# Performance work log

Hardware: AMD Instinct MI355X
Metric: run time of the kernel (lower is better)

## Reference

```python
import jax, jax.numpy as jnp
import numpy as np

N_NODES = 100000
N_EDGES = 1600000
D_IN = 128
D_HID = 128
D_OUT = 64
N_LAYERS = 3
BN_EPS = 1e-5


def _mlp_block(h, W1, b1, g, be, W2, b2):
    # PyG MLP([c_in, h, h]): Linear -> BatchNorm -> ReLU -> Linear (plain last)
    h = h @ W1 + b1                      # [N, h]
    mu = jnp.mean(h, axis=0)
    var = jnp.var(h, axis=0)             # biased var, BN training-mode stats
    h = (h - mu) * jax.lax.rsqrt(var + BN_EPS) * g + be
    h = jax.nn.relu(h)
    return h @ W2 + b2


def setup_inputs() -> dict:
    key = jax.random.key(0)
    ks = jax.random.split(key, 16)
    s_in = 1.0 / np.sqrt(D_IN)
    s_h = 1.0 / np.sqrt(D_HID)
    x = jax.random.normal(ks[0], (N_NODES, D_IN), dtype=jnp.float32)
    edge_index = jax.random.randint(ks[1], (2, N_EDGES), 0, N_NODES, dtype=jnp.int64)
    return {
        "x": x,
        "edge_index": edge_index,
        # stacked per-conv MLP params (all layers are 128->128->128)
        "W1": jax.random.normal(ks[2], (N_LAYERS, D_IN, D_HID), jnp.float32) * s_in,
        "b1": jnp.zeros((N_LAYERS, D_HID), jnp.float32),
        "g1": jnp.ones((N_LAYERS, D_HID), jnp.float32),
        "be1": jnp.zeros((N_LAYERS, D_HID), jnp.float32),
        "W2": jax.random.normal(ks[3], (N_LAYERS, D_HID, D_HID), jnp.float32) * s_h,
        "b2": jnp.zeros((N_LAYERS, D_HID), jnp.float32),
        # final MLP([h, h, out])
        "fW1": jax.random.normal(ks[4], (D_HID, D_HID), jnp.float32) * s_h,
        "fb1": jnp.zeros((D_HID,), jnp.float32),
        "fg1": jnp.ones((D_HID,), jnp.float32),
        "fbe1": jnp.zeros((D_HID,), jnp.float32),
        "fW2": jax.random.normal(ks[5], (D_HID, D_OUT), jnp.float32) * s_h,
        "fb2": jnp.zeros((D_OUT,), jnp.float32),
    }


def reference(x, edge_index, W1, b1, g1, be1, W2, b2, fW1, fb1, fg1, fbe1, fW2, fb2):
    src, dst = edge_index[0], edge_index[1]
    for l in range(N_LAYERS):
        # GINConv, eps=0: nn((1+eps)*x + sum_{j->i} x_j)
        aggr = jax.ops.segment_sum(x[src], dst, num_segments=N_NODES)  # [N, d]
        h = x + aggr
        x = jax.nn.relu(_mlp_block(h, W1[l], b1[l], g1[l], be1[l], W2[l], b2[l]))
    # final MLP (dropout=0.5 is identity in eval mode)
    return _mlp_block(x, fW1, fb1, fg1, fbe1, fW2, fb2)
```

## Files before the change

kernel.cpp:

```cpp
#include <hip/hip_runtime.h>
#include <hip/hip_cooperative_groups.h>

namespace cg = cooperative_groups;

#define NN 100000
#define NE 1600000
#define DD 128
#define CAP 56
#define NGROUP 256

static __device__ __forceinline__ unsigned short f2b(float f) {
  unsigned int x = __float_as_uint(f);
  unsigned int r = x + 0x7fffu + ((x >> 16) & 1u);
  return (unsigned short)(r >> 16);
}
static __device__ __forceinline__ float b2f(unsigned short u) {
  return __uint_as_float(((unsigned int)u) << 16);
}

typedef __attribute__((ext_vector_type(8))) short short8;
typedef __attribute__((ext_vector_type(4))) float f32x4;

union V8 {
  uint4 u4;
  short8 s8;
  unsigned short us[8];
};

__global__ void detect_k(const int* __restrict__ ei, int* __restrict__ flag) {
  int v = ei[2 * threadIdx.x + 1];
  unsigned long long b = __ballot(v != 0);
  if (threadIdx.x == 0) *flag = (b == 0ull) ? 1 : 0;
}

__global__ __launch_bounds__(256) void castpack_k(const float* __restrict__ x,
                                                  unsigned short* __restrict__ x16,
                                                  const int* __restrict__ ei,
                                                  int2* __restrict__ packed,
                                                  int* __restrict__ cnt,
                                                  float* __restrict__ stats,
                                                  const int* __restrict__ flag) {
  const int gid = blockIdx.x * 256 + threadIdx.x;
  size_t i = (size_t)gid * 8;
  f32x4 a = *(const f32x4*)(x + i);
  f32x4 b = *(const f32x4*)(x + i + 4);
  V8 v;
#pragma unroll
  for (int j = 0; j < 4; ++j) {
    v.us[j] = f2b(a[j]);
    v.us[4 + j] = f2b(b[j]);
  }
  *(uint4*)(x16 + i) = v.u4;
  const int mode = *flag;
  int s, d;
  if (mode) {
    s = ((const int2*)ei)[gid].x;
    d = ((const int2*)ei)[(size_t)NE + gid].x;
  } else {
    s = ei[gid];
    d = ei[NE + gid];
  }
  packed[gid] = make_int2(s, d);
  if (gid < NN) cnt[gid] = 0;
  if (gid < 8192) stats[gid] = 0.f;
}

__global__ __launch_bounds__(256) void scatter_k(const int2* __restrict__ packed,
                                                 int* __restrict__ cnt,
                                                 int* __restrict__ csr) {
  const int r = blockIdx.x & 7;
  const int g = blockIdx.x >> 3;
  const int lo = r * (NN / 8), hi = lo + (NN / 8);
  for (int e = g * 256 + threadIdx.x; e < NE; e += NGROUP * 256) {
    int2 sd = packed[e];
    if (sd.y >= lo && sd.y < hi) {
      int c = atomicAdd(&cnt[sd.y], 1);
      if (c < CAP) csr[(size_t)sd.y * CAP + c] = sd.x;
    }
  }
}

__global__ __launch_bounds__(256) void wprep_k(const float* __restrict__ W1,
                                               const float* __restrict__ W2,
                                               const float* __restrict__ fW1,
                                               const float* __restrict__ fW2,
                                               unsigned short* __restrict__ wt) {
  int b = blockIdx.x;
  const float* src;
  int moff, N;
  if (b < 192) {
    int m = b >> 6;
    src = W1 + m * 16384;
    moff = m * 16384;
    N = 128;
    b &= 63;
  } else if (b < 384) {
    int m = (b - 192) >> 6;
    src = W2 + m * 16384;
    moff = (3 + m) * 16384;
    N = 128;
    b = (b - 192) & 63;
  } else if (b < 448) {
    src = fW1;
    moff = 6 * 16384;
    N = 128;
    b -= 384;
  } else {
    src = fW2;
    moff = 7 * 16384;
    N = 64;
    b -= 448;
  }
  int idx = b * 256 + threadIdx.x;
  int n = idx >> 7, k = idx & 127;
  if (n < N) wt[moff + idx] = f2b(src[(size_t)k * N + n]);
}

__global__ __launch_bounds__(256) void gather_k(const int* __restrict__ cnt,
                                                const int* __restrict__ csr,
                                                const unsigned short* __restrict__ x16,
                                                unsigned short* __restrict__ h16) {
  const int node = blockIdx.x * 16 + (threadIdx.x >> 4);
  const int l = threadIdx.x & 15;
  const int beg = node * CAP;
  const int end = beg + cnt[node];
  V8 v;
  v.u4 = *(const uint4*)(x16 + (size_t)node * DD + l * 8);
  float a0[8], a1[8], a2[8], a3[8];
#pragma unroll
  for (int j = 0; j < 8; ++j) {
    a0[j] = b2f(v.us[j]);
    a1[j] = 0.f;
    a2[j] = 0.f;
    a3[j] = 0.f;
  }
  int p = beg;
  for (; p + 4 <= end; p += 4) {
    const int s0 = csr[p], s1 = csr[p + 1], s2 = csr[p + 2], s3 = csr[p + 3];
    V8 w0, w1, w2, w3;
    w0.u4 = *(const uint4*)(x16 + (size_t)s0 * DD + l * 8);
    w1.u4 = *(const uint4*)(x16 + (size_t)s1 * DD + l * 8);
    w2.u4 = *(const uint4*)(x16 + (size_t)s2 * DD + l * 8);
    w3.u4 = *(const uint4*)(x16 + (size_t)s3 * DD + l * 8);
#pragma unroll
    for (int j = 0; j < 8; ++j) {
      a0[j] += b2f(w0.us[j]);
      a1[j] += b2f(w1.us[j]);
      a2[j] += b2f(w2.us[j]);
      a3[j] += b2f(w3.us[j]);
    }
  }
  for (; p < end; ++p) {
    const int s0 = csr[p];
    V8 w0;
    w0.u4 = *(const uint4*)(x16 + (size_t)s0 * DD + l * 8);
#pragma unroll
    for (int j = 0; j < 8; ++j) a0[j] += b2f(w0.us[j]);
  }
  V8 o;
#pragma unroll
  for (int j = 0; j < 8; ++j) o.us[j] = f2b((a0[j] + a1[j]) + (a2[j] + a3[j]));
  *(uint4*)(h16 + (size_t)node * DD + l * 8) = o.u4;
}

template <int SECONDCOLS, int SECEPI>
__global__ __launch_bounds__(512) void layer_k(const unsigned short* __restrict__ Aptr,
                                               const unsigned short* __restrict__ wT1,
                                               const float* __restrict__ bias1,
                                               const unsigned short* __restrict__ wT2,
                                               const float* __restrict__ bias2,
                                               const float* __restrict__ gamma,
                                               const float* __restrict__ beta,
                                               unsigned short* __restrict__ t16,
                                               void* __restrict__ Cptr,
                                               float* __restrict__ stats,
                                               int ntiles) {
  __shared__ unsigned short bT[128][136];
  __shared__ float scS[128];
  __shared__ float shS[128];
  __shared__ float sS[128];
  __shared__ float s2S[128];
  const int tid = threadIdx.x;
  const int wv = tid >> 6;
  const int lane = tid & 63;
  const int l16 = lane & 15;
  const int quad = lane >> 4;

  for (int i = tid; i < 128 * 16; i += 512) {
    int n = i >> 4, k8 = (i & 15) << 3;
    *(uint4*)&bT[n][k8] = *(const uint4*)(wT1 + n * 128 + k8);
  }
  if (tid < 128) {
    sS[tid] = 0.f;
    s2S[tid] = 0.f;
  }
  __syncthreads();

  for (int m = blockIdx.x; m < ntiles; m += gridDim.x) {
    const int arow = m * 128 + wv * 16 + l16;
    const bool rv = arow < NN;
    V8 afr[4];
#pragma unroll
    for (int kc = 0; kc < 4; ++kc) {
      if (rv) {
        afr[kc].u4 = *(const uint4*)(Aptr + (size_t)arow * DD + kc * 32 + quad * 8);
      } else {
        afr[kc].u4 = make_uint4(0u, 0u, 0u, 0u);
      }
    }
    f32x4 acc[8];
#pragma unroll
    for (int nt = 0; nt < 8; ++nt) acc[nt] = (f32x4)(0.0f);
#pragma unroll
    for (int kc = 0; kc < 4; ++kc) {
      const int k0 = kc * 32 + quad * 8;
#pragma unroll
      for (int nt = 0; nt < 8; ++nt) {
        V8 bf;
        bf.u4 = *(const uint4*)&bT[nt * 16 + l16][k0];
        acc[nt] = __builtin_amdgcn_mfma_f32_16x16x32_bf16(afr[kc].s8, bf.s8, acc[nt], 0, 0, 0);
      }
    }
    const int r0 = m * 128 + wv * 16 + quad * 4;
#pragma unroll
    for (int nt = 0; nt < 8; ++nt) {
      const int col = nt * 16 + l16;
      const float bv = bias1[col];
      float s = 0.f, s2 = 0.f;
#pragma unroll
      for (int i = 0; i < 4; ++i) {
        const int r = r0 + i;
        if (r < NN) {
          unsigned short us = f2b(acc[nt][i] + bv);
          t16[(size_t)r * 128 + col] = us;
          float vr = b2f(us);
          s += vr;
          s2 += vr * vr;
        }
      }
      s += __shfl_xor(s, 16);
      s += __shfl_xor(s, 32);
      s2 += __shfl_xor(s2, 16);
      s2 += __shfl_xor(s2, 32);
      if (quad == 0) {
        atomicAdd(&sS[col], s);
        atomicAdd(&s2S[col], s2);
      }
    }
  }
  __syncthreads();
  if (tid < 128) {
    const int xs = (blockIdx.x & 7) * 256;
    atomicAdd(&stats[xs + tid], sS[tid]);
    atomicAdd(&stats[xs + 128 + tid], s2S[tid]);
  }

  cg::this_grid().sync();

  for (int i = tid; i < SECONDCOLS * 16; i += 512) {
    int n = i >> 4, k8 = (i & 15) << 3;
    *(uint4*)&bT[n][k8] = *(const uint4*)(wT2 + n * 128 + k8);
  }
  if (tid < 128) {
    float su = 0.f, sq = 0.f;
#pragma unroll
    for (int j = 0; j < 8; ++j) {
      su += stats[j * 256 + tid];
      sq += stats[j * 256 + 128 + tid];
    }
    const float inv_n = 1.0f / (float)NN;
    float mu = su * inv_n;
    float var = sq * inv_n - mu * mu;
    float sc = gamma[tid] * rsqrtf(var + 1e-5f);
    scS[tid] = sc;
    shS[tid] = beta[tid] - mu * sc;
  }
  __syncthreads();

  for (int m = blockIdx.x; m < ntiles; m += gridDim.x) {
    const int arow = m * 128 + wv * 16 + l16;
    const bool rv = arow < NN;
    V8 afr[4];
#pragma unroll
    for (int kc = 0; kc < 4; ++kc) {
      if (rv) {
        afr[kc].u4 = *(const uint4*)(t16 + (size_t)arow * 128 + kc * 32 + quad * 8);
      } else {
        afr[kc].u4 = make_uint4(0u, 0u, 0u, 0u);
      }
    }
    f32x4 acc[SECONDCOLS / 16];
#pragma unroll
    for (int nt = 0; nt < SECONDCOLS / 16; ++nt) acc[nt] = (f32x4)(0.0f);
#pragma unroll
    for (int kc = 0; kc < 4; ++kc) {
      const int k0 = kc * 32 + quad * 8;
      V8 af = afr[kc];
#pragma unroll
      for (int j = 0; j < 8; ++j) {
        float f = fmaf(b2f(af.us[j]), scS[k0 + j], shS[k0 + j]);
        af.us[j] = f2b(fmaxf(f, 0.0f));
      }
#pragma unroll
      for (int nt = 0; nt < SECONDCOLS / 16; ++nt) {
        V8 bf;
        bf.u4 = *(const uint4*)&bT[nt * 16 + l16][k0];
        acc[nt] = __builtin_amdgcn_mfma_f32_16x16x32_bf16(af.s8, bf.s8, acc[nt], 0, 0, 0);
      }
    }
    const int r0 = m * 128 + wv * 16 + quad * 4;
#pragma unroll
    for (int nt = 0; nt < SECONDCOLS / 16; ++nt) {
      const int col = nt * 16 + l16;
      const float bv = bias2[col];
#pragma unroll
      for (int i = 0; i < 4; ++i) {
        const int r = r0 + i;
        if (r < NN) {
          float v = acc[nt][i] + bv;
          if (SECEPI == 1) {
            ((unsigned short*)Cptr)[(size_t)r * SECONDCOLS + col] = f2b(fmaxf(v, 0.0f));
          } else {
            ((float*)Cptr)[(size_t)r * SECONDCOLS + col] = v;
          }
        }
      }
    }
  }
}

template <int AMODE, int NCOLS, int EPI, int STATS>
__global__ __launch_bounds__(512) void gemm_k(const unsigned short* __restrict__ Aptr,
                                              const unsigned short* __restrict__ wT,
                                              const float* __restrict__ bias,
                                              const float* __restrict__ bn_stats,
                                              const float* __restrict__ gamma,
                                              const float* __restrict__ beta,
                                              void* __restrict__ Cptr,
                                              float* __restrict__ stats_out) {
  __shared__ unsigned short bT[NCOLS][136];
  __shared__ float biasS[NCOLS];
  __shared__ float scS[128];
  __shared__ float shS[128];
  __shared__ float sS[NCOLS];
  __shared__ float s2S[NCOLS];
  const int tid = threadIdx.x;
  const int wv = tid >> 6;
  const int lane = tid & 63;
  const int l16 = lane & 15;
  const int quad = lane >> 4;
  const int arow = blockIdx.x * 128 + wv * 16 + l16;
  const bool rv = arow < NN;

  V8 afr[4];
#pragma unroll
  for (int kc = 0; kc < 4; ++kc) {
    if (rv) {
      afr[kc].u4 = *(const uint4*)(Aptr + (size_t)arow * DD + kc * 32 + quad * 8);
    } else {
      afr[kc].u4 = make_uint4(0u, 0u, 0u, 0u);
    }
  }
  for (int i = tid; i < NCOLS * 16; i += 512) {
    int n = i >> 4, k8 = (i & 15) << 3;
    *(uint4*)&bT[n][k8] = *(const uint4*)(wT + n * 128 + k8);
  }
  if (tid < NCOLS) biasS[tid] = bias[tid];
  if (AMODE == 2 && tid < 128) {
    float su = 0.f, sq = 0.f;
#pragma unroll
    for (int j = 0; j < 8; ++j) {
      su += bn_stats[j * 256 + tid];
      sq += bn_stats[j * 256 + 128 + tid];
    }
    const float inv_n = 1.0f / (float)NN;
    float mu = su * inv_n;
    float var = sq * inv_n - mu * mu;
    float sc = gamma[tid] * rsqrtf(var + 1e-5f);
    scS[tid] = sc;
    shS[tid] = beta[tid] - mu * sc;
  }
  if (STATS && tid < NCOLS) {
    sS[tid] = 0.f;
    s2S[tid] = 0.f;
  }
  __syncthreads();

  f32x4 acc[NCOLS / 16];
#pragma unroll
  for (int nt = 0; nt < NCOLS / 16; ++nt) acc[nt] = (f32x4)(0.0f);
#pragma unroll
  for (int kc = 0; kc < 4; ++kc) {
    const int k0 = kc * 32 + quad * 8;
    V8 af = afr[kc];
    if (AMODE == 2) {
#pragma unroll
      for (int j = 0; j < 8; ++j) {
        float f = fmaf(b2f(af.us[j]), scS[k0 + j], shS[k0 + j]);
        af.us[j] = f2b(fmaxf(f, 0.0f));
      }
    }
#pragma unroll
    for (int nt = 0; nt < NCOLS / 16; ++nt) {
      V8 bf;
      bf.u4 = *(const uint4*)&bT[nt * 16 + l16][k0];
      acc[nt] = __builtin_amdgcn_mfma_f32_16x16x32_bf16(af.s8, bf.s8, acc[nt], 0, 0, 0);
    }
  }
  const int r0 = blockIdx.x * 128 + wv * 16 + quad * 4;
#pragma unroll
  for (int nt = 0; nt < NCOLS / 16; ++nt) {
    const int col = nt * 16 + l16;
    const float bv = biasS[col];
    float s = 0.f, s2 = 0.f;
#pragma unroll
    for (int i = 0; i < 4; ++i) {
      const int r = r0 + i;
      if (r < NN) {
        float v = acc[nt][i] + bv;
        if (EPI == 1) v = fmaxf(v, 0.0f);
        if (EPI == 2) {
          ((float*)Cptr)[(size_t)r * NCOLS + col] = v;
        } else {
          unsigned short us = f2b(v);
          ((unsigned short*)Cptr)[(size_t)r * NCOLS + col] = us;
          if (STATS) {
            float vr = b2f(us);
            s += vr;
            s2 += vr * vr;
          }
        }
      }
    }
    if (STATS) {
      s += __shfl_xor(s, 16);
      s += __shfl_xor(s, 32);
      s2 += __shfl_xor(s2, 16);
      s2 += __shfl_xor(s2, 32);
      if (quad == 0) {
        atomicAdd(&sS[col], s);
        atomicAdd(&s2S[col], s2);
      }
    }
  }
  if (STATS) {
    __syncthreads();
    if (tid < NCOLS) {
      const int xs = (blockIdx.x & 7) * 256;
      atomicAdd(&stats_out[xs + tid], sS[tid]);
      atomicAdd(&stats_out[xs + 128 + tid], s2S[tid]);
    }
  }
}

extern "C" void kernel_launch(void* const* d_in, const int* in_sizes, int n_in,
                              void* d_out, int out_size, void* d_ws, size_t ws_size,
                              hipStream_t stream) {
  const float* x = (const float*)d_in[0];
  const int* ei = (const int*)d_in[1];
  const float* W1 = (const float*)d_in[2];
  const float* b1 = (const float*)d_in[3];
  const float* g1 = (const float*)d_in[4];
  const float* be1 = (const float*)d_in[5];
  const float* W2 = (const float*)d_in[6];
  const float* b2 = (const float*)d_in[7];
  const float* fW1 = (const float*)d_in[8];
  const float* fb1 = (const float*)d_in[9];
  const float* fg1 = (const float*)d_in[10];
  const float* fbe1 = (const float*)d_in[11];
  const float* fW2 = (const float*)d_in[12];
  const float* fb2 = (const float*)d_in[13];

  char* ws = (char*)d_ws;
  unsigned short* x16 = (unsigned short*)ws;
  unsigned short* h16 = (unsigned short*)(ws + (size_t)25600000);
  unsigned short* t16 = (unsigned short*)(ws + (size_t)51200000);
  int2* packed = (int2*)t16;
  int* csr = (int*)(ws + (size_t)76800000);
  int* cnt = (int*)(ws + (size_t)99200000);
  float* stats = (float*)(ws + (size_t)99600000);
  int* flag = (int*)(ws + (size_t)99632896);
  unsigned short* wt = (unsigned short*)(ws + (size_t)99634176);

  const int vecBlocks = (NN * DD) / (256 * 8);
  const int gemmBlocks = (NN + 127) / 128;
  const int filtBlocks = NGROUP * 8;
  const int nodeBlocks = NN / 16;

  int dev = 0, coop = 0;
  hipGetDevice(&dev);
  hipDeviceGetAttribute(&coop, hipDeviceAttributeCooperativeLaunch, dev);
  int occA = 0, occB = 0;
  hipOccupancyMaxActiveBlocksPerMultiprocessor(&occA, layer_k<128, 1>, 512, 0);
  hipOccupancyMaxActiveBlocksPerMultiprocessor(&occB, layer_k<64, 2>, 512, 0);
  int gridA = occA > 0 ? occA * 256 : 0;
  int gridB = occB > 0 ? occB * 256 : 0;
  if (gridA > gemmBlocks) gridA = gemmBlocks;
  if (gridB > gemmBlocks) gridB = gemmBlocks;
  const bool useCoop = (coop != 0) && (gridA > 0) && (gridB > 0);

  detect_k<<<1, 64, 0, stream>>>(ei, flag);
  castpack_k<<<vecBlocks, 256, 0, stream>>>(x, x16, ei, packed, cnt, stats, flag);
  wprep_k<<<480, 256, 0, stream>>>(W1, W2, fW1, fW2, wt);
  scatter_k<<<filtBlocks, 256, 0, stream>>>(packed, cnt, csr);

  int ntiles = gemmBlocks;
  for (int l = 0; l < 3; ++l) {
    gather_k<<<nodeBlocks, 256, 0, stream>>>(cnt, csr, x16, h16);
    if (useCoop) {
      const unsigned short* Ap = h16;
      const unsigned short* w1p = wt + (size_t)l * 16384;
      const float* b1p = b1 + l * 128;
      const unsigned short* w2p = wt + (size_t)(3 + l) * 16384;
      const float* b2p = b2 + l * 128;
      const float* gp = g1 + l * 128;
      const float* bep = be1 + l * 128;
      unsigned short* tp = t16;
      void* cp = (void*)x16;
      float* sp = stats + 2048 * l;
      void* args[] = {&Ap, &w1p, &b1p, &w2p, &b2p, &gp, &bep, &tp, &cp, &sp, &ntiles};
      hipLaunchCooperativeKernel((void*)layer_k<128, 1>, dim3(gridA), dim3(512),
                                 args, 0, stream);
    } else {
      gemm_k<1, 128, 0, 1><<<gemmBlocks, 512, 0, stream>>>(
          h16, wt + (size_t)l * 16384, b1 + l * 128, nullptr, nullptr, nullptr,
          t16, stats + 2048 * l);
      gemm_k<2, 128, 1, 0><<<gemmBlocks, 512, 0, stream>>>(
          t16, wt + (size_t)(3 + l) * 16384, b2 + l * 128, stats + 2048 * l,
          g1 + l * 128, be1 + l * 128, x16, nullptr);
    }
  }

  if (useCoop) {
    const unsigned short* Ap = x16;
    const unsigned short* w1p = wt + (size_t)6 * 16384;
    const float* b1p = fb1;
    const unsigned short* w2p = wt + (size_t)7 * 16384;
    const float* b2p = fb2;
    const float* gp = fg1;
    const float* bep = fbe1;
    unsigned short* tp = t16;
    void* cp = d_out;
    float* sp = stats + 6144;
    void* args[] = {&Ap, &w1p, &b1p, &w2p, &b2p, &gp, &bep, &tp, &cp, &sp, &ntiles};
    hipLaunchCooperativeKernel((void*)layer_k<64, 2>, dim3(gridB), dim3(512),
                               args, 0, stream);
  } else {
    gemm_k<1, 128, 0, 1><<<gemmBlocks, 512, 0, stream>>>(
        x16, wt + (size_t)6 * 16384, fb1, nullptr, nullptr, nullptr, t16,
        stats + 6144);
    gemm_k<2, 64, 2, 0><<<gemmBlocks, 512, 0, stream>>>(
        t16, wt + (size_t)7 * 16384, fb2, stats + 6144, fg1, fbe1, (float*)d_out,
        nullptr);
  }
}
```

Before: 555.3 us.

## Fuse dtype detection and weight prep into castpack, widen gather unroll, stripe stats

Result: no change. 551.5 us (-0.7%).

```diff
diff --git a/kernel.cpp b/kernel.cpp
--- a/kernel.cpp
+++ b/kernel.cpp
@@ -8,6 +8,7 @@
 #define DD 128
 #define CAP 56
 #define NGROUP 256
+#define NSTRIPE 32
 
 static __device__ __forceinline__ unsigned short f2b(float f) {
   unsigned int x = __float_as_uint(f);
@@ -26,12 +27,6 @@
   short8 s8;
   unsigned short us[8];
 };
-
-__global__ void detect_k(const int* __restrict__ ei, int* __restrict__ flag) {
-  int v = ei[2 * threadIdx.x + 1];
-  unsigned long long b = __ballot(v != 0);
-  if (threadIdx.x == 0) *flag = (b == 0ull) ? 1 : 0;
-}
 
 __global__ __launch_bounds__(256) void castpack_k(const float* __restrict__ x,
                                                   unsigned short* __restrict__ x16,
@@ -39,8 +34,22 @@
                                                   int2* __restrict__ packed,
                                                   int* __restrict__ cnt,
                                                   float* __restrict__ stats,
-                                                  const int* __restrict__ flag) {
-  const int gid = blockIdx.x * 256 + threadIdx.x;
+                                                  const float* __restrict__ W1,
+                                                  const float* __restrict__ W2,
+                                                  const float* __restrict__ fW1,
+                                                  const float* __restrict__ fW2,
+                                                  unsigned short* __restrict__ wt) {
+  __shared__ int modeS;
+  const int tid = threadIdx.x;
+  if (tid < 64) {
+    int v = ei[2 * tid + 1];
+    unsigned long long b = __ballot(v != 0);
+    if (tid == 0) modeS = (b == 0ull) ? 1 : 0;
+  }
+  __syncthreads();
+  const int mode = modeS;
+  const int gid = blockIdx.x * 256 + tid;
+
   size_t i = (size_t)gid * 8;
   f32x4 a = *(const f32x4*)(x + i);
   f32x4 b = *(const f32x4*)(x + i + 4);
@@ -51,7 +60,7 @@
     v.us[4 + j] = f2b(b[j]);
   }
   *(uint4*)(x16 + i) = v.u4;
-  const int mode = *flag;
+
   int s, d;
   if (mode) {
     s = ((const int2*)ei)[gid].x;
@@ -62,7 +71,39 @@
   }
   packed[gid] = make_int2(s, d);
   if (gid < NN) cnt[gid] = 0;
-  if (gid < 8192) stats[gid] = 0.f;
+  if (gid < 4 * NSTRIPE * 256) stats[gid] = 0.f;
+
+  if (blockIdx.x < 480) {
+    int bb = blockIdx.x;
+    const float* src;
+    int moff, N;
+    if (bb < 192) {
+      int m = bb >> 6;
+      src = W1 + m * 16384;
+      moff = m * 16384;
+      N = 128;
+      bb &= 63;
+    } else if (bb < 384) {
+      int m = (bb - 192) >> 6;
+      src = W2 + m * 16384;
+      moff = (3 + m) * 16384;
+      N = 128;
+      bb = (bb - 192) & 63;
+    } else if (bb < 448) {
+      src = fW1;
+      moff = 6 * 16384;
+      N = 128;
+      bb -= 384;
+    } else {
+      src = fW2;
+      moff = 7 * 16384;
+      N = 64;
+      bb -= 448;
+    }
+    int idx = bb * 256 + tid;
+    int n = idx >> 7, k = idx & 127;
+    if (n < N) wt[moff + idx] = f2b(src[(size_t)k * N + n]);
+  }
 }
 
 __global__ __launch_bounds__(256) void scatter_k(const int2* __restrict__ packed,
@@ -80,42 +121,6 @@
   }
 }
 
-__global__ __launch_bounds__(256) void wprep_k(const float* __restrict__ W1,
-                                               const float* __restrict__ W2,
-                                               const float* __restrict__ fW1,
-                                               const float* __restrict__ fW2,
-                                               unsigned short* __restrict__ wt) {
-  int b = blockIdx.x;
-  const float* src;
-  int moff, N;
-  if (b < 192) {
-    int m = b >> 6;
-    src = W1 + m * 16384;
-    moff = m * 16384;
-    N = 128;
-    b &= 63;
-  } else if (b < 384) {
-    int m = (b - 192) >> 6;
-    src = W2 + m * 16384;
-    moff = (3 + m) * 16384;
-    N = 128;
-    b = (b - 192) & 63;
-  } else if (b < 448) {
-    src = fW1;
-    moff = 6 * 16384;
-    N = 128;
-    b -= 384;
-  } else {
-    src = fW2;
-    moff = 7 * 16384;
-    N = 64;
-    b -= 448;
-  }
-  int idx = b * 256 + threadIdx.x;
-  int n = idx >> 7, k = idx & 127;
-  if (n < N) wt[moff + idx] = f2b(src[(size_t)k * N + n]);
-}
-
 __global__ __launch_bounds__(256) void gather_k(const int* __restrict__ cnt,
                                                 const int* __restrict__ csr,
                                                 const unsigned short* __restrict__ x16,
@@ -126,40 +131,52 @@
   const int end = beg + cnt[node];
   V8 v;
   v.u4 = *(const uint4*)(x16 + (size_t)node * DD + l * 8);
-  float a0[8], a1[8], a2[8], a3[8];
+  float ac0[8], ac1[8];
 #pragma unroll
   for (int j = 0; j < 8; ++j) {
-    a0[j] = b2f(v.us[j]);
-    a1[j] = 0.f;
-    a2[j] = 0.f;
-    a3[j] = 0.f;
+    ac0[j] = b2f(v.us[j]);
+    ac1[j] = 0.f;
   }
   int p = beg;
-  for (; p + 4 <= end; p += 4) {
+  for (; p + 8 <= end; p += 8) {
     const int s0 = csr[p], s1 = csr[p + 1], s2 = csr[p + 2], s3 = csr[p + 3];
-    V8 w0, w1, w2, w3;
+    const int s4 = csr[p + 4], s5 = csr[p + 5], s6 = csr[p + 6], s7 = csr[p + 7];
+    V8 w0, w1, w2, w3, w4, w5, w6, w7;
     w0.u4 = *(const uint4*)(x16 + (size_t)s0 * DD + l * 8);
     w1.u4 = *(const uint4*)(x16 + (size_t)s1 * DD + l * 8);
     w2.u4 = *(const uint4*)(x16 + (size_t)s2 * DD + l * 8);
     w3.u4 = *(const uint4*)(x16 + (size_t)s3 * DD + l * 8);
+    w4.u4 = *(const uint4*)(x16 + (size_t)s4 * DD + l * 8);
+    w5.u4 = *(const uint4*)(x16 + (size_t)s5 * DD + l * 8);
+    w6.u4 = *(const uint4*)(x16 + (size_t)s6 * DD + l * 8);
+    w7.u4 = *(const uint4*)(x16 + (size_t)s7 * DD + l * 8);
 #pragma unroll
     for (int j = 0; j < 8; ++j) {
-      a0[j] += b2f(w0.us[j]);
-      a1[j] += b2f(w1.us[j]);
-      a2[j] += b2f(w2.us[j]);
-      a3[j] += b2f(w3.us[j]);
-    }
-  }
-  for (; p < end; ++p) {
+      ac0[j] += (b2f(w0.us[j]) + b2f(w2.us[j])) + (b2f(w4.us[j]) + b2f(w6.us[j]));
+      ac1[j] += (b2f(w1.us[j]) + b2f(w3.us[j])) + (b2f(w5.us[j]) + b2f(w7.us[j]));
+    }
+  }
+  for (; p + 2 <= end; p += 2) {
+    const int s0 = csr[p], s1 = csr[p + 1];
+    V8 w0, w1;
+    w0.u4 = *(const uint4*)(x16 + (size_t)s0 * DD + l * 8);
+    w1.u4 = *(const uint4*)(x16 + (size_t)s1 * DD + l * 8);
+#pragma unroll
+    for (int j = 0; j < 8; ++j) {
+      ac0[j] += b2f(w0.us[j]);
+      ac1[j] += b2f(w1.us[j]);
+    }
+  }
+  if (p < end) {
     const int s0 = csr[p];
     V8 w0;
     w0.u4 = *(const uint4*)(x16 + (size_t)s0 * DD + l * 8);
 #pragma unroll
-    for (int j = 0; j < 8; ++j) a0[j] += b2f(w0.us[j]);
+    for (int j = 0; j < 8; ++j) ac0[j] += b2f(w0.us[j]);
   }
   V8 o;
 #pragma unroll
-  for (int j = 0; j < 8; ++j) o.us[j] = f2b((a0[j] + a1[j]) + (a2[j] + a3[j]));
+  for (int j = 0; j < 8; ++j) o.us[j] = f2b(ac0[j] + ac1[j]);
   *(uint4*)(h16 + (size_t)node * DD + l * 8) = o.u4;
 }
 
@@ -250,7 +267,7 @@
   }
   __syncthreads();
   if (tid < 128) {
-    const int xs = (blockIdx.x & 7) * 256;
+    const int xs = (blockIdx.x & (NSTRIPE - 1)) * 256;
     atomicAdd(&stats[xs + tid], sS[tid]);
     atomicAdd(&stats[xs + 128 + tid], s2S[tid]);
   }
@@ -264,7 +281,7 @@
   if (tid < 128) {
     float su = 0.f, sq = 0.f;
 #pragma unroll
-    for (int j = 0; j < 8; ++j) {
+    for (int j = 0; j < NSTRIPE; ++j) {
       su += stats[j * 256 + tid];
       sq += stats[j * 256 + 128 + tid];
     }
@@ -369,7 +386,7 @@
   if (AMODE == 2 && tid < 128) {
     float su = 0.f, sq = 0.f;
 #pragma unroll
-    for (int j = 0; j < 8; ++j) {
+    for (int j = 0; j < NSTRIPE; ++j) {
       su += bn_stats[j * 256 + tid];
       sq += bn_stats[j * 256 + 128 + tid];
     }
@@ -446,7 +463,7 @@
   if (STATS) {
     __syncthreads();
     if (tid < NCOLS) {
-      const int xs = (blockIdx.x & 7) * 256;
+      const int xs = (blockIdx.x & (NSTRIPE - 1)) * 256;
       atomicAdd(&stats_out[xs + tid], sS[tid]);
       atomicAdd(&stats_out[xs + 128 + tid], s2S[tid]);
     }
@@ -479,8 +496,7 @@
   int* csr = (int*)(ws + (size_t)76800000);
   int* cnt = (int*)(ws + (size_t)99200000);
   float* stats = (float*)(ws + (size_t)99600000);
-  int* flag = (int*)(ws + (size_t)99632896);
-  unsigned short* wt = (unsigned short*)(ws + (size_t)99634176);
+  unsigned short* wt = (unsigned short*)(ws + (size_t)99731072);
 
   const int vecBlocks = (NN * DD) / (256 * 8);
   const int gemmBlocks = (NN + 127) / 128;
@@ -499,9 +515,8 @@
   if (gridB > gemmBlocks) gridB = gemmBlocks;
   const bool useCoop = (coop != 0) && (gridA > 0) && (gridB > 0);
 
-  detect_k<<<1, 64, 0, stream>>>(ei, flag);
-  castpack_k<<<vecBlocks, 256, 0, stream>>>(x, x16, ei, packed, cnt, stats, flag);
-  wprep_k<<<480, 256, 0, stream>>>(W1, W2, fW1, fW2, wt);
+  castpack_k<<<vecBlocks, 256, 0, stream>>>(x, x16, ei, packed, cnt, stats, W1,
+                                            W2, fW1, fW2, wt);
   scatter_k<<<filtBlocks, 256, 0, stream>>>(packed, cnt, csr);
 
   int ntiles = gemmBlocks;
@@ -517,16 +532,16 @@
       const float* bep = be1 + l * 128;
       unsigned short* tp = t16;
       void* cp = (void*)x16;
-      float* sp = stats + 2048 * l;
+      float* sp = stats + 256 * NSTRIPE * l;
       void* args[] = {&Ap, &w1p, &b1p, &w2p, &b2p, &gp, &bep, &tp, &cp, &sp, &ntiles};
       hipLaunchCooperativeKernel((void*)layer_k<128, 1>, dim3(gridA), dim3(512),
                                  args, 0, stream);
     } else {
       gemm_k<1, 128, 0, 1><<<gemmBlocks, 512, 0, stream>>>(
           h16, wt + (size_t)l * 16384, b1 + l * 128, nullptr, nullptr, nullptr,
-          t16, stats + 2048 * l);
+          t16, stats + 256 * NSTRIPE * l);
       gemm_k<2, 128, 1, 0><<<gemmBlocks, 512, 0, stream>>>(
-          t16, wt + (size_t)(3 + l) * 16384, b2 + l * 128, stats + 2048 * l,
+          t16, wt + (size_t)(3 + l) * 16384, b2 + l * 128, stats + 256 * NSTRIPE * l,
           g1 + l * 128, be1 + l * 128, x16, nullptr);
     }
   }
@@ -541,16 +556,16 @@
     const float* bep = fbe1;
     unsigned short* tp = t16;
     void* cp = d_out;
-    float* sp = stats + 6144;
+    float* sp = stats + 256 * NSTRIPE * 3;
     void* args[] = {&Ap, &w1p, &b1p, &w2p, &b2p, &gp, &bep, &tp, &cp, &sp, &ntiles};
     hipLaunchCooperativeKernel((void*)layer_k<64, 2>, dim3(gridB), dim3(512),
                                args, 0, stream);
   } else {
     gemm_k<1, 128, 0, 1><<<gemmBlocks, 512, 0, stream>>>(
         x16, wt + (size_t)6 * 16384, fb1, nullptr, nullptr, nullptr, t16,
-        stats + 6144);
+        stats + 256 * NSTRIPE * 3);
     gemm_k<2, 64, 2, 0><<<gemmBlocks, 512, 0, stream>>>(
-        t16, wt + (size_t)7 * 16384, fb2, stats + 6144, fg1, fbe1, (float*)d_out,
-        nullptr);
-  }
-}
+        t16, wt + (size_t)7 * 16384, fb2, stats + 256 * NSTRIPE * 3, fg1, fbe1,
+        (float*)d_out, nullptr);
+  }
+}
```
